# Optimization experiments

Measured on AMD Instinct MI355X. Metric: run time of the kernel, lower is better.

Reference implementation:

```python
import jax, jax.numpy as jnp
import numpy as np

NEG_SLOPE = 0.2


def gat_conv(x, edge_index, W, a_src, a_dst, b):
    # PyG GATConv (heads=1, add_self_loops=True, concat -> out_channels)
    N = x.shape[0]
    h = x @ W                                   # [N, F_out]
    loops = jnp.arange(N, dtype=edge_index.dtype)
    src = jnp.concatenate([edge_index[0], loops])   # message sources (x_j)
    dst = jnp.concatenate([edge_index[1], loops])   # message targets (x_i)
    # attention logits: e = LeakyReLU(a_src . h_j + a_dst . h_i)
    alpha_s = h @ a_src                          # [N]
    alpha_d = h @ a_dst                          # [N]
    e = jax.nn.leaky_relu(alpha_s[src] + alpha_d[dst], NEG_SLOPE)  # [E+N]
    # segment softmax over incoming edges of each dst node
    m = jax.ops.segment_max(e, dst, num_segments=N)
    e = jnp.exp(e - m[dst])
    denom = jax.ops.segment_sum(e, dst, num_segments=N)
    alpha = e / denom[dst]                       # self-loops guarantee denom > 0
    # weighted scatter-sum aggregation
    out = jax.ops.segment_sum(alpha[:, None] * h[src], dst, num_segments=N)
    return out + b


def setup_inputs() -> dict:
    key = jax.random.key(0)
    ks = jax.random.split(key, 10)
    N, E, F_in, H, F_out = 100000, 3200000, 54, 16, 16
    x = jax.random.normal(ks[0], (N, F_in), dtype=jnp.float32)
    edge_index = jax.random.randint(ks[1], (2, E), 0, N, dtype=jnp.int64)
    s1 = 1.0 / np.sqrt(F_in)
    s2 = 1.0 / np.sqrt(H)
    return {
        "x": x,
        "edge_index": edge_index,
        "W1": jax.random.uniform(ks[2], (F_in, H), jnp.float32, -s1, s1),
        "a1_src": jax.random.uniform(ks[3], (H,), jnp.float32, -s2, s2),
        "a1_dst": jax.random.uniform(ks[4], (H,), jnp.float32, -s2, s2),
        "b1": jnp.zeros((H,), jnp.float32),
        "W2": jax.random.uniform(ks[5], (H, F_out), jnp.float32, -s2, s2),
        "a2_src": jax.random.uniform(ks[6], (F_out,), jnp.float32, -0.25, 0.25),
        "a2_dst": jax.random.uniform(ks[7], (F_out,), jnp.float32, -0.25, 0.25),
        "b2": jnp.zeros((F_out,), jnp.float32),
    }


def reference(x, edge_index, W1, a1_src, a1_dst, b1, W2, a2_src, a2_dst, b2):
    h = gat_conv(x, edge_index, W1, a1_src, a1_dst, b1)
    h = jax.nn.elu(h)
    # dropout p=0.5 is identity in eval mode
    out = gat_conv(h, edge_index, W2, a2_src, a2_dst, b2)
    return out
```

## Files before the change

### kernel.cpp

```cpp
#include <hip/hip_runtime.h>
#include <hip/hip_bf16.h>

typedef __hip_bfloat16 bf16;

static constexpr int N_NODES = 100000;
static constexpr int N_EDGES = 3200000;
static constexpr int F_IN    = 54;
static constexpr int F_HID   = 16;

static constexpr int BSHIFT    = 7;
static constexpr int BNODES    = 128;
static constexpr int NBUCK     = (N_NODES + BNODES - 1) / BNODES;
static constexpr int CAP_B     = 5120;
static constexpr int BIN_CHUNK = 8192;
static constexpr int GRDB      = (N_EDGES + BIN_CHUNK - 1) / BIN_CHUNK;
static constexpr int GRDN_F    = (N_NODES + 1023) / 1024;

static constexpr size_t WS_FLAGS  = 0;
static constexpr size_t WS_ADST   = 4;
static constexpr size_t WS_ADST2  = 100004;
static constexpr size_t WS_BCNT   = 200004;
static constexpr size_t WS_ROWBEG = 201028;
static constexpr size_t WS_ROWCNT = 301028;
static constexpr size_t WS_HC1    = 401028;
static constexpr size_t WS_HC2    = 2001028;
static constexpr size_t WS_BEDGES = 3601028;
static constexpr size_t WS_SRCS   = 7604868;
static constexpr size_t WS_BUCKET_END = WS_SRCS + (size_t)NBUCK * CAP_B;
static constexpr size_t WS_FB_DEN     = 3601028;
static constexpr size_t WS_FB_AS      = 3701028;
static constexpr size_t WS_ATOMIC_END = 3801028;

__device__ __forceinline__ float lrelu(float v) { return v >= 0.f ? v : 0.2f * v; }
__device__ __forceinline__ float loadf(const void* p, int i, bool f32) {
    return f32 ? ((const float*)p)[i] : __bfloat162float(((const bf16*)p)[i]);
}
__device__ __forceinline__ unsigned f2bf(float f) {
    unsigned u = __float_as_uint(f);
    return (u + 0x7FFFu + ((u >> 16) & 1u)) >> 16;
}

__global__ __launch_bounds__(256) void k_probe0(
    const void* __restrict__ x, const void* __restrict__ ei,
    int* __restrict__ flags, int* __restrict__ bcnt)
{
    __shared__ int cnt, nz;
    const int t = threadIdx.x;
    if (t == 0) { cnt = 0; nz = 0; }
    __syncthreads();
    const unsigned u = ((const unsigned*)x)[t];
    if ((u & 0x7FFFu) >= 0x4800u) atomicAdd(&cnt, 1);
    if (t < 64) {
        if (((const unsigned*)ei)[2 * t + 1] != 0u) atomicAdd(&nz, 1);
    }
    for (int i = t; i < 1024; i += 256) bcnt[i] = 0;
    __syncthreads();
    if (t == 0) flags[0] = ((cnt >= 16) ? 1 : 0) | ((nz == 0) ? 2 : 0);
}

__global__ __launch_bounds__(1024, 8) void k_binfeat(
    const void* __restrict__ ei, const void* __restrict__ x,
    const void* __restrict__ W1, const void* __restrict__ a_s,
    const void* __restrict__ a_d, const int* __restrict__ flags,
    int* __restrict__ bcnt, int* __restrict__ bedges,
    unsigned* __restrict__ hc, float* __restrict__ adst)
{
    __shared__ int            hist[NBUCK];
    __shared__ int            base[NBUCK];
    __shared__ int            cval[BIN_CHUNK];
    __shared__ unsigned short cbkt[BIN_CHUNK];
    __shared__ float Wl[F_IN * F_HID];
    __shared__ float asl[F_HID];
    __shared__ float adl[F_HID];
    const int t = threadIdx.x;
    const bool f32 = flags[0] & 1;
    const bool i64 = flags[0] & 2;

    if (blockIdx.x < GRDB) {
        const int e0 = blockIdx.x * BIN_CHUNK;
        const int valid = min(BIN_CHUNK, N_EDGES - e0);
        for (int i = t; i < NBUCK; i += 1024) hist[i] = 0;
        __syncthreads();
#pragma unroll
        for (int i = 0; i < BIN_CHUNK / 1024; ++i) {
            const int idx = i * 1024 + t;
            const int e = e0 + idx;
            if (idx < valid) {
                int s, d;
                if (i64) {
                    s = ((const int*)ei)[2 * (size_t)e];
                    d = ((const int*)ei)[2 * ((size_t)N_EDGES + e)];
                } else {
                    s = ((const int*)ei)[e];
                    d = ((const int*)ei)[(size_t)N_EDGES + e];
                }
                const int b = d >> BSHIFT;
                cval[idx] = (s << BSHIFT) | (d & (BNODES - 1));
                cbkt[idx] = (unsigned short)b;
                atomicAdd(&hist[b], 1);
            }
        }
        __syncthreads();
        for (int i = t; i < NBUCK; i += 1024) {
            const int c = hist[i];
            base[i] = c ? atomicAdd(&bcnt[i], c) : 0;
            hist[i] = 0;
        }
        __syncthreads();
#pragma unroll
        for (int i = 0; i < BIN_CHUNK / 1024; ++i) {
            const int idx = i * 1024 + t;
            if (idx < valid) {
                const int b = cbkt[idx];
                const int r = atomicAdd(&hist[b], 1);
                const int pos = base[b] + r;
                if (pos < CAP_B) bedges[(size_t)b * CAP_B + pos] = cval[idx];
            }
        }
    } else {
        for (int i = t; i < F_IN * F_HID; i += 1024) Wl[i] = loadf(W1, i, f32);
        if (t < F_HID) { asl[t] = loadf(a_s, t, f32); adl[t] = loadf(a_d, t, f32); }
        __syncthreads();
        const int node = (blockIdx.x - GRDB) * 1024 + t;
        if (node >= N_NODES) return;

        float h[F_HID];
#pragma unroll
        for (int k = 0; k < F_HID; ++k) h[k] = 0.f;
        if (f32) {
            const float2* xp = (const float2*)((const float*)x + (size_t)node * F_IN);
#pragma unroll
            for (int j = 0; j < F_IN / 2; ++j) {
                const float2 v = xp[j];
#pragma unroll
                for (int k = 0; k < F_HID; ++k) {
                    h[k] = fmaf(v.x, Wl[(2*j)   * F_HID + k], h[k]);
                    h[k] = fmaf(v.y, Wl[(2*j+1) * F_HID + k], h[k]);
                }
            }
        } else {
            const unsigned* xu = (const unsigned*)x + (size_t)node * (F_IN / 2);
#pragma unroll
            for (int j = 0; j < F_IN / 2; ++j) {
                const unsigned u = xu[j];
                const float v0 = __uint_as_float(u << 16);
                const float v1 = __uint_as_float(u & 0xFFFF0000u);
#pragma unroll
                for (int k = 0; k < F_HID; ++k) {
                    h[k] = fmaf(v0, Wl[(2*j)   * F_HID + k], h[k]);
                    h[k] = fmaf(v1, Wl[(2*j+1) * F_HID + k], h[k]);
                }
            }
        }
        float s = 0.f, d = 0.f;
#pragma unroll
        for (int k = 0; k < F_HID; ++k) { s = fmaf(h[k], asl[k], s); d = fmaf(h[k], adl[k], d); }
        adst[node] = d;
        const unsigned ab = f2bf(s) << 16;
        unsigned pk[F_HID];
#pragma unroll
        for (int k = 0; k < F_HID; ++k) pk[k] = f2bf(h[k]) | ab;
        uint4* hb = (uint4*)(hc + (size_t)node * F_HID);
#pragma unroll
        for (int q = 0; q < 4; ++q)
            hb[q] = make_uint4(pk[4*q], pk[4*q+1], pk[4*q+2], pk[4*q+3]);
    }
}

__global__ __launch_bounds__(512) void k_bsort(
    const int* __restrict__ bcnt, const int* __restrict__ bedges,
    int* __restrict__ rowbeg, int* __restrict__ rowcnt, int* __restrict__ srcs)
{
    __shared__ int hist[BNODES];
    __shared__ int scan[BNODES];
    __shared__ int cur[BNODES];
    const int t = threadIdx.x;
    const int b = blockIdx.x;
    const int n0 = b << BSHIFT;
    if (t < BNODES) hist[t] = 0;
    __syncthreads();
    const int cnt = min(bcnt[b], CAP_B);
    const int* be = bedges + (size_t)b * CAP_B;
    for (int e = t; e < cnt; e += 512)
        atomicAdd(&hist[be[e] & (BNODES - 1)], 1);
    __syncthreads();
    if (t < BNODES) scan[t] = (hist[t] + 3) & ~3;
    __syncthreads();
#pragma unroll
    for (int off = 1; off < BNODES; off <<= 1) {
        const int v = (t < BNODES && t >= off) ? scan[t - off] : 0;
        __syncthreads();
        if (t < BNODES) scan[t] += v;
        __syncthreads();
    }
    if (t < BNODES) {
        const int ex = scan[t] - ((hist[t] + 3) & ~3);
        cur[t] = ex;
        const int node = n0 + t;
        if (node < N_NODES) {
            rowbeg[node] = b * CAP_B + ex;
            rowcnt[node] = hist[t];
        }
    }
    __syncthreads();
    for (int e = t; e < cnt; e += 512) {
        const int p = be[e];
        const int dl = p & (BNODES - 1);
        const int r = atomicAdd(&cur[dl], 1);
        if (r < CAP_B) srcs[(size_t)b * CAP_B + r] = p >> BSHIFT;
    }
}

__global__ __launch_bounds__(256) void k_agg1(
    const int* __restrict__ rowbeg, const int* __restrict__ rowcnt,
    const int* __restrict__ srcs, const float* __restrict__ adst,
    const unsigned* __restrict__ hc, const void* __restrict__ b1,
    const void* __restrict__ W2, const void* __restrict__ a_s2,
    const void* __restrict__ a_d2, const int* __restrict__ flags,
    unsigned* __restrict__ hc2, float* __restrict__ adst2)
{
    __shared__ float Wl[F_HID * F_HID];
    __shared__ float asl[F_HID];
    __shared__ float adl[F_HID];
    __shared__ float bl[F_HID];
    const bool f32 = flags[0] & 1;
    const int t = threadIdx.x;
    if (t < F_HID * F_HID) Wl[t] = loadf(W2, t, f32);
    if (t < F_HID) {
        asl[t] = loadf(a_s2, t, f32);
        adl[t] = loadf(a_d2, t, f32);
        bl[t]  = loadf(b1, t, f32);
    }
    __syncthreads();

    const int k = t & 15;
    const int node = blockIdx.x * 16 + (t >> 4);
    const float adn = adst[node];
    const unsigned vs = hc[(size_t)node * F_HID + k];
    const float w0 = __expf(lrelu(__uint_as_float(vs & 0xFFFF0000u) + adn));
    float denom = w0;
    float acc = w0 * __uint_as_float(vs << 16);
    const int n = rowcnt[node];
    const int* sp = srcs + rowbeg[node];
    int i = 0;
    for (; i + 8 <= n; i += 8) {
        const int4 sa = *(const int4*)(sp + i);
        const int4 sb = *(const int4*)(sp + i + 4);
        const unsigned v0 = hc[(size_t)sa.x * F_HID + k];
        const unsigned v1 = hc[(size_t)sa.y * F_HID + k];
        const unsigned v2 = hc[(size_t)sa.z * F_HID + k];
        const unsigned v3 = hc[(size_t)sa.w * F_HID + k];
        const unsigned v4 = hc[(size_t)sb.x * F_HID + k];
        const unsigned v5 = hc[(size_t)sb.y * F_HID + k];
        const unsigned v6 = hc[(size_t)sb.z * F_HID + k];
        const unsigned v7 = hc[(size_t)sb.w * F_HID + k];
        const float e0 = __expf(lrelu(__uint_as_float(v0 & 0xFFFF0000u) + adn));
        const float e1 = __expf(lrelu(__uint_as_float(v1 & 0xFFFF0000u) + adn));
        const float e2 = __expf(lrelu(__uint_as_float(v2 & 0xFFFF0000u) + adn));
        const float e3 = __expf(lrelu(__uint_as_float(v3 & 0xFFFF0000u) + adn));
        const float e4 = __expf(lrelu(__uint_as_float(v4 & 0xFFFF0000u) + adn));
        const float e5 = __expf(lrelu(__uint_as_float(v5 & 0xFFFF0000u) + adn));
        const float e6 = __expf(lrelu(__uint_as_float(v6 & 0xFFFF0000u) + adn));
        const float e7 = __expf(lrelu(__uint_as_float(v7 & 0xFFFF0000u) + adn));
        denom += (e0 + e1 + e2 + e3) + (e4 + e5 + e6 + e7);
        acc = fmaf(e0, __uint_as_float(v0 << 16), acc);
        acc = fmaf(e1, __uint_as_float(v1 << 16), acc);
        acc = fmaf(e2, __uint_as_float(v2 << 16), acc);
        acc = fmaf(e3, __uint_as_float(v3 << 16), acc);
        acc = fmaf(e4, __uint_as_float(v4 << 16), acc);
        acc = fmaf(e5, __uint_as_float(v5 << 16), acc);
        acc = fmaf(e6, __uint_as_float(v6 << 16), acc);
        acc = fmaf(e7, __uint_as_float(v7 << 16), acc);
    }
    for (; i < n; ++i) {
        const unsigned v = hc[(size_t)sp[i] * F_HID + k];
        const float w = __expf(lrelu(__uint_as_float(v & 0xFFFF0000u) + adn));
        denom += w;
        acc = fmaf(w, __uint_as_float(v << 16), acc);
    }
    float z = acc / denom + bl[k];
    z = z > 0.f ? z : expm1f(z);

    float hh = 0.f;
#pragma unroll
    for (int j = 0; j < F_HID; ++j) {
        const float zj = __shfl(z, j, 16);
        hh = fmaf(zj, Wl[j * F_HID + k], hh);
    }
    float s2 = hh * asl[k], d2 = hh * adl[k];
#pragma unroll
    for (int off = 1; off < 16; off <<= 1) {
        s2 += __shfl_xor(s2, off, 16);
        d2 += __shfl_xor(d2, off, 16);
    }
    hc2[(size_t)node * F_HID + k] = f2bf(hh) | (f2bf(s2) << 16);
    if (k == 0) adst2[node] = d2;
}

__global__ __launch_bounds__(256) void k_agg2(
    const int* __restrict__ rowbeg, const int* __restrict__ rowcnt,
    const int* __restrict__ srcs, const float* __restrict__ adst,
    const unsigned* __restrict__ hc, const void* __restrict__ b2,
    const int* __restrict__ flags, float* __restrict__ outp)
{
    const bool f32 = flags[0] & 1;
    const int t = threadIdx.x;
    const int k = t & 15;
    const int node = blockIdx.x * 16 + (t >> 4);
    const float adn = adst[node];
    const unsigned vs = hc[(size_t)node * F_HID + k];
    const float w0 = __expf(lrelu(__uint_as_float(vs & 0xFFFF0000u) + adn));
    float denom = w0;
    float acc = w0 * __uint_as_float(vs << 16);
    const int n = rowcnt[node];
    const int* sp = srcs + rowbeg[node];
    int i = 0;
    for (; i + 8 <= n; i += 8) {
        const int4 sa = *(const int4*)(sp + i);
        const int4 sb = *(const int4*)(sp + i + 4);
        const unsigned v0 = hc[(size_t)sa.x * F_HID + k];
        const unsigned v1 = hc[(size_t)sa.y * F_HID + k];
        const unsigned v2 = hc[(size_t)sa.z * F_HID + k];
        const unsigned v3 = hc[(size_t)sa.w * F_HID + k];
        const unsigned v4 = hc[(size_t)sb.x * F_HID + k];
        const unsigned v5 = hc[(size_t)sb.y * F_HID + k];
        const unsigned v6 = hc[(size_t)sb.z * F_HID + k];
        const unsigned v7 = hc[(size_t)sb.w * F_HID + k];
        const float e0 = __expf(lrelu(__uint_as_float(v0 & 0xFFFF0000u) + adn));
        const float e1 = __expf(lrelu(__uint_as_float(v1 & 0xFFFF0000u) + adn));
        const float e2 = __expf(lrelu(__uint_as_float(v2 & 0xFFFF0000u) + adn));
        const float e3 = __expf(lrelu(__uint_as_float(v3 & 0xFFFF0000u) + adn));
        const float e4 = __expf(lrelu(__uint_as_float(v4 & 0xFFFF0000u) + adn));
        const float e5 = __expf(lrelu(__uint_as_float(v5 & 0xFFFF0000u) + adn));
        const float e6 = __expf(lrelu(__uint_as_float(v6 & 0xFFFF0000u) + adn));
        const float e7 = __expf(lrelu(__uint_as_float(v7 & 0xFFFF0000u) + adn));
        denom += (e0 + e1 + e2 + e3) + (e4 + e5 + e6 + e7);
        acc = fmaf(e0, __uint_as_float(v0 << 16), acc);
        acc = fmaf(e1, __uint_as_float(v1 << 16), acc);
        acc = fmaf(e2, __uint_as_float(v2 << 16), acc);
        acc = fmaf(e3, __uint_as_float(v3 << 16), acc);
        acc = fmaf(e4, __uint_as_float(v4 << 16), acc);
        acc = fmaf(e5, __uint_as_float(v5 << 16), acc);
        acc = fmaf(e6, __uint_as_float(v6 << 16), acc);
        acc = fmaf(e7, __uint_as_float(v7 << 16), acc);
    }
    for (; i < n; ++i) {
        const unsigned v = hc[(size_t)sp[i] * F_HID + k];
        const float w = __expf(lrelu(__uint_as_float(v & 0xFFFF0000u) + adn));
        denom += w;
        acc = fmaf(w, __uint_as_float(v << 16), acc);
    }
    outp[(size_t)node * F_HID + k] = acc / denom + loadf(b2, k, f32);
}

__global__ __launch_bounds__(256) void k_feat1(
    const void* __restrict__ x, const void* __restrict__ W1,
    const void* __restrict__ a_s, const void* __restrict__ a_d,
    const int* __restrict__ flags,
    float* __restrict__ hbuf, float* __restrict__ asrc, float* __restrict__ adst)
{
    const bool f32 = flags[0] & 1;
    __shared__ float Wl[F_IN * F_HID];
    __shared__ float asl[F_HID];
    __shared__ float adl[F_HID];
    const int t = threadIdx.x;
    for (int i = t; i < F_IN * F_HID; i += 256) Wl[i] = loadf(W1, i, f32);
    if (t < F_HID) { asl[t] = loadf(a_s, t, f32); adl[t] = loadf(a_d, t, f32); }
    __syncthreads();
    const int node = blockIdx.x * 256 + t;
    if (node >= N_NODES) return;
    float h[F_HID];
#pragma unroll
    for (int k = 0; k < F_HID; ++k) h[k] = 0.f;
    if (f32) {
        const float2* xp = (const float2*)((const float*)x + (size_t)node * F_IN);
#pragma unroll
        for (int j = 0; j < F_IN / 2; ++j) {
            const float2 v = xp[j];
#pragma unroll
            for (int k = 0; k < F_HID; ++k) {
                h[k] = fmaf(v.x, Wl[(2*j)   * F_HID + k], h[k]);
                h[k] = fmaf(v.y, Wl[(2*j+1) * F_HID + k], h[k]);
            }
        }
    } else {
        const unsigned* xu = (const unsigned*)x + (size_t)node * (F_IN / 2);
#pragma unroll
        for (int j = 0; j < F_IN / 2; ++j) {
            const unsigned u = xu[j];
            const float v0 = __uint_as_float(u << 16);
            const float v1 = __uint_as_float(u & 0xFFFF0000u);
#pragma unroll
            for (int k = 0; k < F_HID; ++k) {
                h[k] = fmaf(v0, Wl[(2*j)   * F_HID + k], h[k]);
                h[k] = fmaf(v1, Wl[(2*j+1) * F_HID + k], h[k]);
            }
        }
    }
    float s = 0.f, d = 0.f;
#pragma unroll
    for (int k = 0; k < F_HID; ++k) { s = fmaf(h[k], asl[k], s); d = fmaf(h[k], adl[k], d); }
    asrc[node] = s; adst[node] = d;
    float4* hb = (float4*)(hbuf + (size_t)node * F_HID);
#pragma unroll
    for (int q = 0; q < 4; ++q)
        hb[q] = make_float4(h[4*q], h[4*q+1], h[4*q+2], h[4*q+3]);
}

__global__ __launch_bounds__(256) void k_selfinit(
    const float* __restrict__ asrc, const float* __restrict__ adst,
    const float* __restrict__ h, float* __restrict__ denom, float* __restrict__ acc)
{
    const int t = blockIdx.x * 256 + threadIdx.x;
    if (t >= N_NODES * F_HID) return;
    const int n = t >> 4;
    const float w0 = __expf(lrelu(asrc[n] + adst[n]));
    if ((t & 15) == 0) denom[n] = w0;
    acc[t] = w0 * h[t];
}

__global__ __launch_bounds__(256) void k_edge(
    const void* __restrict__ ei, const int* __restrict__ flags,
    const float* __restrict__ asrc, const float* __restrict__ adst,
    const float* __restrict__ hbuf,
    float* __restrict__ denom, float* __restrict__ acc)
{
    const int e = blockIdx.x * 256 + threadIdx.x;
    if (e >= N_EDGES) return;
    int s, d;
    if (flags[0] & 2) {
        const long long* e64 = (const long long*)ei;
        s = (int)e64[e]; d = (int)e64[(size_t)N_EDGES + e];
    } else {
        const int* e32 = (const int*)ei;
        s = e32[e]; d = e32[(size_t)N_EDGES + e];
    }
    const float w = __expf(lrelu(asrc[s] + adst[d]));
    atomicAdd(&denom[d], w);
    const float4* hs = (const float4*)(hbuf + (size_t)s * F_HID);
    float* ad = acc + (size_t)d * F_HID;
#pragma unroll
    for (int q = 0; q < 4; ++q) {
        const float4 hv = hs[q];
        atomicAdd(ad + 4*q + 0, w * hv.x);
        atomicAdd(ad + 4*q + 1, w * hv.y);
        atomicAdd(ad + 4*q + 2, w * hv.z);
        atomicAdd(ad + 4*q + 3, w * hv.w);
    }
}

__global__ __launch_bounds__(256) void k_div_elu(
    float* __restrict__ acc, const float* __restrict__ denom,
    const void* __restrict__ b1, const int* __restrict__ flags)
{
    const bool f32 = flags[0] & 1;
    const int t = blockIdx.x * 256 + threadIdx.x;
    if (t >= N_NODES * F_HID) return;
    const float v = acc[t] / denom[t >> 4] + loadf(b1, t & 15, f32);
    acc[t] = v > 0.f ? v : expm1f(v);
}

__global__ __launch_bounds__(256) void k_mid(
    const float* __restrict__ z,
    const void* __restrict__ W2, const void* __restrict__ a_s2,
    const void* __restrict__ a_d2, const int* __restrict__ flags,
    float* __restrict__ h2, float* __restrict__ asrc, float* __restrict__ adst)
{
    const bool f32 = flags[0] & 1;
    __shared__ float Wl[F_HID * F_HID];
    __shared__ float asl[F_HID];
    __shared__ float adl[F_HID];
    const int t = threadIdx.x;
    if (t < F_HID * F_HID) Wl[t] = loadf(W2, t, f32);
    if (t < F_HID) { asl[t] = loadf(a_s2, t, f32); adl[t] = loadf(a_d2, t, f32); }
    __syncthreads();
    const int node = blockIdx.x * 256 + t;
    if (node >= N_NODES) return;
    float zr[F_HID];
    const float4* zi = (const float4*)(z + (size_t)node * F_HID);
#pragma unroll
    for (int q = 0; q < 4; ++q) {
        const float4 zv = zi[q];
        zr[4*q+0]=zv.x; zr[4*q+1]=zv.y; zr[4*q+2]=zv.z; zr[4*q+3]=zv.w;
    }
    float h[F_HID];
#pragma unroll
    for (int k = 0; k < F_HID; ++k) h[k] = 0.f;
#pragma unroll
    for (int j = 0; j < F_HID; ++j) {
        const float zv = zr[j];
#pragma unroll
        for (int k = 0; k < F_HID; ++k) h[k] = fmaf(zv, Wl[j * F_HID + k], h[k]);
    }
    float s = 0.f, d = 0.f;
#pragma unroll
    for (int k = 0; k < F_HID; ++k) { s = fmaf(h[k], asl[k], s); d = fmaf(h[k], adl[k], d); }
    asrc[node] = s; adst[node] = d;
    float4* hb = (float4*)(h2 + (size_t)node * F_HID);
#pragma unroll
    for (int q = 0; q < 4; ++q)
        hb[q] = make_float4(h[4*q], h[4*q+1], h[4*q+2], h[4*q+3]);
}

__global__ __launch_bounds__(256) void k_out(
    const float* __restrict__ acc, const float* __restrict__ denom,
    const void* __restrict__ b2, const int* __restrict__ flags,
    float* __restrict__ out)
{
    const bool f32 = flags[0] & 1;
    const int t = blockIdx.x * 256 + threadIdx.x;
    if (t >= N_NODES * F_HID) return;
    out[t] = acc[t] / denom[t >> 4] + loadf(b2, t & 15, f32);
}

__global__ __launch_bounds__(256) void k_diag(float* __restrict__ out, float v)
{
    const int t = blockIdx.x * 256 + threadIdx.x;
    if (t < N_NODES * F_HID) out[t] = v;
}

extern "C" void kernel_launch(void* const* d_in, const int* in_sizes, int n_in,
                              void* d_out, int out_size, void* d_ws, size_t ws_size,
                              hipStream_t stream) {
    const void* x   = d_in[0];
    const void* ei  = d_in[1];
    const void* W1  = d_in[2];
    const void* a1s = d_in[3];
    const void* a1d = d_in[4];
    const void* b1  = d_in[5];
    const void* W2  = d_in[6];
    const void* a2s = d_in[7];
    const void* a2d = d_in[8];
    const void* b2  = d_in[9];
    float* out = (float*)d_out;

    float* ws = (float*)d_ws;
    int*      flags  = (int*)(ws + WS_FLAGS);
    float*    adst   = ws + WS_ADST;
    float*    adst2  = ws + WS_ADST2;
    int*      bcnt   = (int*)(ws + WS_BCNT);
    int*      rowbeg = (int*)(ws + WS_ROWBEG);
    int*      rowcnt = (int*)(ws + WS_ROWCNT);
    unsigned* hc1    = (unsigned*)(ws + WS_HC1);
    unsigned* hc2    = (unsigned*)(ws + WS_HC2);
    int*      bedges = (int*)(ws + WS_BEDGES);
    int*      srcs   = (int*)(ws + WS_SRCS);

    const dim3 blk(256);
    const dim3 grdN((N_NODES + 255) / 256);
    const dim3 grdE((N_EDGES + 255) / 256);
    const dim3 grdO((N_NODES * F_HID + 255) / 256);
    const dim3 grdBF(GRDB + GRDN_F);
    const dim3 grdS(NBUCK);
    const dim3 grdA(N_NODES / 16);

    if (ws_size >= WS_BUCKET_END * 4) {
        k_probe0 <<<dim3(1), blk, 0, stream>>>(x, ei, flags, bcnt);
        k_binfeat<<<grdBF, dim3(1024), 0, stream>>>(ei, x, W1, a1s, a1d, flags,
                                                    bcnt, bedges, hc1, adst);
        k_bsort  <<<grdS, dim3(512), 0, stream>>>(bcnt, bedges, rowbeg, rowcnt, srcs);
        k_agg1   <<<grdA, blk, 0, stream>>>(rowbeg, rowcnt, srcs, adst, hc1,
                                            b1, W2, a2s, a2d, flags, hc2, adst2);
        k_agg2   <<<grdA, blk, 0, stream>>>(rowbeg, rowcnt, srcs, adst2, hc2,
                                            b2, flags, out);
    } else if (ws_size >= WS_ATOMIC_END * 4) {
        float* fb_h   = ws + WS_HC1;
        float* fb_acc = ws + WS_HC2;
        float* fb_den = ws + WS_FB_DEN;
        float* fb_as  = ws + WS_FB_AS;
        float* fb_ad  = ws + WS_ADST;
        k_probe0 <<<dim3(1), blk, 0, stream>>>(x, ei, flags, bcnt);
        k_feat1  <<<grdN, blk, 0, stream>>>(x, W1, a1s, a1d, flags, fb_h, fb_as, fb_ad);
        k_selfinit<<<grdO, blk, 0, stream>>>(fb_as, fb_ad, fb_h, fb_den, fb_acc);
        k_edge   <<<grdE, blk, 0, stream>>>(ei, flags, fb_as, fb_ad, fb_h, fb_den, fb_acc);
        k_div_elu<<<grdO, blk, 0, stream>>>(fb_acc, fb_den, b1, flags);
        k_mid    <<<grdN, blk, 0, stream>>>(fb_acc, W2, a2s, a2d, flags, fb_h, fb_as, fb_ad);
        k_selfinit<<<grdO, blk, 0, stream>>>(fb_as, fb_ad, fb_h, fb_den, fb_acc);
        k_edge   <<<grdE, blk, 0, stream>>>(ei, flags, fb_as, fb_ad, fb_h, fb_den, fb_acc);
        k_out    <<<grdO, blk, 0, stream>>>(fb_acc, fb_den, b2, flags, out);
    } else {
        k_diag<<<grdO, blk, 0, stream>>>(out, (float)(ws_size >> 10));
    }
}
```

Measured before the change: 266.1 us.

## Share per-edge attention exp across lanes via shuffles and store byte offsets

In both aggregation kernels, each 16-lane group now splits a 16-edge chunk so that every lane loads one source index and computes one exp. The index and weight are then broadcast with shuffles, so the 16 lanes no longer each recompute the same exp and reload the same indices. The CSR source array now stores precomputed byte offsets (index shifted by 6), which removes the address multiply in the gather. LeakyReLU becomes a fmax. The cost is 32 extra shuffles per 16 edges, and the per-edge gathers are still serialized.

```diff
diff --git a/kernel.cpp b/kernel.cpp
--- a/kernel.cpp
+++ b/kernel.cpp
@@ -31,7 +31,7 @@
 static constexpr size_t WS_FB_AS      = 3701028;
 static constexpr size_t WS_ATOMIC_END = 3801028;
 
-__device__ __forceinline__ float lrelu(float v) { return v >= 0.f ? v : 0.2f * v; }
+__device__ __forceinline__ float lrelu(float v) { return fmaxf(v, 0.2f * v); }
 __device__ __forceinline__ float loadf(const void* p, int i, bool f32) {
     return f32 ? ((const float*)p)[i] : __bfloat162float(((const bf16*)p)[i]);
 }
@@ -207,7 +207,7 @@
         const int p = be[e];
         const int dl = p & (BNODES - 1);
         const int r = atomicAdd(&cur[dl], 1);
-        if (r < CAP_B) srcs[(size_t)b * CAP_B + r] = p >> BSHIFT;
+        if (r < CAP_B) srcs[(size_t)b * CAP_B + r] = (p >> BSHIFT) << 6;
     }
 }
 
@@ -236,6 +236,7 @@
     const int k = t & 15;
     const int node = blockIdx.x * 16 + (t >> 4);
     const float adn = adst[node];
+    const char* hcb = (const char*)hc + 4 * k;
     const unsigned vs = hc[(size_t)node * F_HID + k];
     const float w0 = __expf(lrelu(__uint_as_float(vs & 0xFFFF0000u) + adn));
     float denom = w0;
@@ -243,37 +244,22 @@
     const int n = rowcnt[node];
     const int* sp = srcs + rowbeg[node];
     int i = 0;
-    for (; i + 8 <= n; i += 8) {
-        const int4 sa = *(const int4*)(sp + i);
-        const int4 sb = *(const int4*)(sp + i + 4);
-        const unsigned v0 = hc[(size_t)sa.x * F_HID + k];
-        const unsigned v1 = hc[(size_t)sa.y * F_HID + k];
-        const unsigned v2 = hc[(size_t)sa.z * F_HID + k];
-        const unsigned v3 = hc[(size_t)sa.w * F_HID + k];
-        const unsigned v4 = hc[(size_t)sb.x * F_HID + k];
-        const unsigned v5 = hc[(size_t)sb.y * F_HID + k];
-        const unsigned v6 = hc[(size_t)sb.z * F_HID + k];
-        const unsigned v7 = hc[(size_t)sb.w * F_HID + k];
-        const float e0 = __expf(lrelu(__uint_as_float(v0 & 0xFFFF0000u) + adn));
-        const float e1 = __expf(lrelu(__uint_as_float(v1 & 0xFFFF0000u) + adn));
-        const float e2 = __expf(lrelu(__uint_as_float(v2 & 0xFFFF0000u) + adn));
-        const float e3 = __expf(lrelu(__uint_as_float(v3 & 0xFFFF0000u) + adn));
-        const float e4 = __expf(lrelu(__uint_as_float(v4 & 0xFFFF0000u) + adn));
-        const float e5 = __expf(lrelu(__uint_as_float(v5 & 0xFFFF0000u) + adn));
-        const float e6 = __expf(lrelu(__uint_as_float(v6 & 0xFFFF0000u) + adn));
-        const float e7 = __expf(lrelu(__uint_as_float(v7 & 0xFFFF0000u) + adn));
-        denom += (e0 + e1 + e2 + e3) + (e4 + e5 + e6 + e7);
-        acc = fmaf(e0, __uint_as_float(v0 << 16), acc);
-        acc = fmaf(e1, __uint_as_float(v1 << 16), acc);
-        acc = fmaf(e2, __uint_as_float(v2 << 16), acc);
-        acc = fmaf(e3, __uint_as_float(v3 << 16), acc);
-        acc = fmaf(e4, __uint_as_float(v4 << 16), acc);
-        acc = fmaf(e5, __uint_as_float(v5 << 16), acc);
-        acc = fmaf(e6, __uint_as_float(v6 << 16), acc);
-        acc = fmaf(e7, __uint_as_float(v7 << 16), acc);
+    for (; i + 16 <= n; i += 16) {
+        const unsigned off = (unsigned)sp[i + k];
+        const unsigned vown = *(const unsigned*)(hcb + off);
+        const float eo = __expf(lrelu(__uint_as_float(vown & 0xFFFF0000u) + adn));
+#pragma unroll
+        for (int m = 0; m < 16; ++m) {
+            const unsigned om = (unsigned)__shfl((int)off, m, 16);
+            const float   em = __shfl(eo, m, 16);
+            const unsigned v = *(const unsigned*)(hcb + om);
+            denom += em;
+            acc = fmaf(em, __uint_as_float(v << 16), acc);
+        }
     }
     for (; i < n; ++i) {
-        const unsigned v = hc[(size_t)sp[i] * F_HID + k];
+        const unsigned off = (unsigned)sp[i];
+        const unsigned v = *(const unsigned*)(hcb + off);
         const float w = __expf(lrelu(__uint_as_float(v & 0xFFFF0000u) + adn));
         denom += w;
         acc = fmaf(w, __uint_as_float(v << 16), acc);
@@ -308,6 +294,7 @@
     const int k = t & 15;
     const int node = blockIdx.x * 16 + (t >> 4);
     const float adn = adst[node];
+    const char* hcb = (const char*)hc + 4 * k;
     const unsigned vs = hc[(size_t)node * F_HID + k];
     const float w0 = __expf(lrelu(__uint_as_float(vs & 0xFFFF0000u) + adn));
     float denom = w0;
@@ -315,37 +302,22 @@
     const int n = rowcnt[node];
     const int* sp = srcs + rowbeg[node];
     int i = 0;
-    for (; i + 8 <= n; i += 8) {
-        const int4 sa = *(const int4*)(sp + i);
-        const int4 sb = *(const int4*)(sp + i + 4);
-        const unsigned v0 = hc[(size_t)sa.x * F_HID + k];
-        const unsigned v1 = hc[(size_t)sa.y * F_HID + k];
-        const unsigned v2 = hc[(size_t)sa.z * F_HID + k];
-        const unsigned v3 = hc[(size_t)sa.w * F_HID + k];
-        const unsigned v4 = hc[(size_t)sb.x * F_HID + k];
-        const unsigned v5 = hc[(size_t)sb.y * F_HID + k];
-        const unsigned v6 = hc[(size_t)sb.z * F_HID + k];
-        const unsigned v7 = hc[(size_t)sb.w * F_HID + k];
-        const float e0 = __expf(lrelu(__uint_as_float(v0 & 0xFFFF0000u) + adn));
-        const float e1 = __expf(lrelu(__uint_as_float(v1 & 0xFFFF0000u) + adn));
-        const float e2 = __expf(lrelu(__uint_as_float(v2 & 0xFFFF0000u) + adn));
-        const float e3 = __expf(lrelu(__uint_as_float(v3 & 0xFFFF0000u) + adn));
-        const float e4 = __expf(lrelu(__uint_as_float(v4 & 0xFFFF0000u) + adn));
-        const float e5 = __expf(lrelu(__uint_as_float(v5 & 0xFFFF0000u) + adn));
-        const float e6 = __expf(lrelu(__uint_as_float(v6 & 0xFFFF0000u) + adn));
-        const float e7 = __expf(lrelu(__uint_as_float(v7 & 0xFFFF0000u) + adn));
-        denom += (e0 + e1 + e2 + e3) + (e4 + e5 + e6 + e7);
-        acc = fmaf(e0, __uint_as_float(v0 << 16), acc);
-        acc = fmaf(e1, __uint_as_float(v1 << 16), acc);
-        acc = fmaf(e2, __uint_as_float(v2 << 16), acc);
-        acc = fmaf(e3, __uint_as_float(v3 << 16), acc);
-        acc = fmaf(e4, __uint_as_float(v4 << 16), acc);
-        acc = fmaf(e5, __uint_as_float(v5 << 16), acc);
-        acc = fmaf(e6, __uint_as_float(v6 << 16), acc);
-        acc = fmaf(e7, __uint_as_float(v7 << 16), acc);
+    for (; i + 16 <= n; i += 16) {
+        const unsigned off = (unsigned)sp[i + k];
+        const unsigned vown = *(const unsigned*)(hcb + off);
+        const float eo = __expf(lrelu(__uint_as_float(vown & 0xFFFF0000u) + adn));
+#pragma unroll
+        for (int m = 0; m < 16; ++m) {
+            const unsigned om = (unsigned)__shfl((int)off, m, 16);
+            const float   em = __shfl(eo, m, 16);
+            const unsigned v = *(const unsigned*)(hcb + om);
+            denom += em;
+            acc = fmaf(em, __uint_as_float(v << 16), acc);
+        }
     }
     for (; i < n; ++i) {
-        const unsigned v = hc[(size_t)sp[i] * F_HID + k];
+        const unsigned off = (unsigned)sp[i];
+        const unsigned v = *(const unsigned*)(hcb + off);
         const float w = __expf(lrelu(__uint_as_float(v & 0xFFFF0000u) + adn));
         denom += w;
         acc = fmaf(w, __uint_as_float(v << 16), acc);
```

Result: slower. 314.2 us (+18.1%).
